# Optimization experiments

Hardware: AMD Instinct MI355X
Metric: run time of the kernel (lower is better)

Reference implementation:

```python
import jax, jax.numpy as jnp
import numpy as np

HEAD_DIM = 256
N_Q = 8
N_KV = 4
HIDDEN = 2304
WINDOW = 1024
SOFT_CAP = 50.0
MAX_WAVELENGTH = 10000.0


def _rope(x, start_index=0):
    # x: [b, s, n, h]. keras_hub RotaryEmbedding (rotate-half convention),
    # followed by Gemma's interleave permutation of the feature dim.
    b, s, n, h = x.shape
    inv_freq = 1.0 / (MAX_WAVELENGTH ** (jnp.arange(0, h, 2, dtype=jnp.float32) / h))
    pos = jnp.arange(s, dtype=jnp.float32) + start_index
    freq = pos[:, None] * inv_freq[None, :]            # [s, h/2]
    emb = jnp.concatenate([freq, freq], axis=-1)[None, :, None, :]  # [1, s, 1, h]
    cos, sin = jnp.cos(emb).astype(x.dtype), jnp.sin(emb).astype(x.dtype)
    x1, x2 = jnp.split(x, 2, axis=-1)
    rot = jnp.concatenate([-x2, x1], axis=-1)
    y = x * cos + rot * sin
    # Gemma _apply_rope: split halves then interleave (same permutation on q and k)
    a, b2 = jnp.split(y, 2, axis=-1)
    return jnp.stack([a, b2], axis=-1).reshape(x.shape)


def setup_inputs() -> dict:
    key = jax.random.key(0)
    ks = jax.random.split(key, 5)
    B, T, D = 2, 2048, HIDDEN
    x = jax.random.normal(ks[0], (B, T, D), dtype=jnp.float32)
    # causal mask [b, q_len, kv_len]
    causal = jnp.tril(jnp.ones((T, T), dtype=bool))
    attention_mask = jnp.broadcast_to(causal[None], (B, T, T))
    scale = 0.02
    Wq = jax.random.normal(ks[1], (N_Q, D, HEAD_DIM), dtype=jnp.float32) * scale
    Wk = jax.random.normal(ks[2], (N_KV, D, HEAD_DIM), dtype=jnp.float32) * scale
    Wv = jax.random.normal(ks[3], (N_KV, D, HEAD_DIM), dtype=jnp.float32) * scale
    Wo = jax.random.normal(ks[4], (N_Q, HEAD_DIM, D), dtype=jnp.float32) * scale
    return {"x": x, "attention_mask": attention_mask, "Wq": Wq, "Wk": Wk, "Wv": Wv, "Wo": Wo}


def reference(x, attention_mask, Wq, Wk, Wv, Wo):
    b, t, d = x.shape
    q = jnp.einsum('btd,ndh->btnh', x, Wq)
    k = jnp.einsum('bsd,kdh->bskh', x, Wk)
    v = jnp.einsum('bsd,kdh->bskh', x, Wv)
    q = _rope(q)
    k = _rope(k)
    s = k.shape[1]
    # sliding window band mask (triu(-w+1) & tril(w-1)), rows sliced at cache_update_index=0
    i = jnp.arange(s)[:, None]
    j = jnp.arange(s)[None, :]
    sliding = (j - i <= WINDOW - 1) & (i - j <= WINDOW - 1)
    mask = attention_mask & sliding[None, :t, :s]      # [b, t, s]
    q = q * jnp.asarray(1.0 / np.sqrt(HEAD_DIM), dtype=q.dtype)
    g = N_Q // N_KV
    qg = q.reshape(b, t, N_KV, g, HEAD_DIM)
    logits = jnp.einsum('btkgh,bskh->bkgts', qg, k).astype(jnp.float32)
    logits = jnp.tanh(logits / SOFT_CAP) * SOFT_CAP    # logit soft-cap
    m = mask[:, None, None, :, :]                      # [b, 1, 1, t, s]
    logits = jnp.where(m, logits, jnp.float32(-1e30))
    probs = jax.nn.softmax(logits, axis=-1).astype(q.dtype)
    out = jnp.einsum('bkgts,bskh->btkgh', probs, v).reshape(b, t, N_Q, HEAD_DIM)
    no_attended = jnp.all(~attention_mask, axis=-1, keepdims=True)[..., None]  # [b, t, 1, 1]
    out = jnp.where(no_attended, jnp.zeros_like(out), out)
    return jnp.einsum('btnh,nhd->btd', out, Wo)
```

## Files before the change

### kernel.cpp

```cpp
#include <hip/hip_runtime.h>
#include <math.h>

#define HEAD_DIM 256
#define N_Q 8
#define N_KV 4
#define HIDDEN 2304
#define WINDOW 1024
#define BATCH 2
#define SEQ 2048
#define BT (BATCH*SEQ)

typedef unsigned short u16;
typedef __attribute__((ext_vector_type(8))) short bf16x8;
typedef __attribute__((ext_vector_type(4))) float f32x4;

__device__ __forceinline__ u16 f2bf(float f) {
    union { float f; unsigned u; } c; c.f = f;
    unsigned r = c.u + 0x7FFF + ((c.u >> 16) & 1);
    return (u16)(r >> 16);
}
__device__ __forceinline__ float bf2f(u16 b) {
    union { float f; unsigned u; } c; c.u = ((unsigned)b) << 16;
    return c.f;
}

__global__ __launch_bounds__(256) void convert_x_kernel(
    const float* __restrict__ x, u16* __restrict__ xb, int n8)
{
    int i = blockIdx.x * 256 + threadIdx.x;
    if (i >= n8) return;
    const float4 a = ((const float4*)x)[2*i];
    const float4 b = ((const float4*)x)[2*i+1];
    u16 o[8] = { f2bf(a.x), f2bf(a.y), f2bf(a.z), f2bf(a.w),
                 f2bf(b.x), f2bf(b.y), f2bf(b.z), f2bf(b.w) };
    ((uint4*)xb)[i] = *(const uint4*)o;
}

__global__ __launch_bounds__(256) void wqkv_t_kernel(
    const float* __restrict__ Wq, const float* __restrict__ Wk,
    const float* __restrict__ Wv, u16* __restrict__ Wt)
{
    __shared__ float t[64][65];
    const int j = blockIdx.z;
    const float* W = (j < 8)  ? Wq + (size_t)j*HIDDEN*HEAD_DIM
                   : (j < 12) ? Wk + (size_t)(j-8)*HIDDEN*HEAD_DIM
                              : Wv + (size_t)(j-12)*HIDDEN*HEAD_DIM;
    const int d0 = blockIdx.x * 64, h0 = blockIdx.y * 64;
    const int tid = threadIdx.x;
    {
        const int r = tid >> 4, c4 = tid & 15;
        #pragma unroll
        for (int rr = r; rr < 64; rr += 16) {
            const float4 v = *(const float4*)(W + (size_t)(d0+rr)*HEAD_DIM + h0 + c4*4);
            t[rr][c4*4+0] = v.x; t[rr][c4*4+1] = v.y;
            t[rr][c4*4+2] = v.z; t[rr][c4*4+3] = v.w;
        }
    }
    __syncthreads();
    {
        const int hh = tid >> 2;
        #pragma unroll
        for (int it = 0; it < 2; it++) {
            const int chunk = (tid & 3) + it*4;
            u16 tmp[8];
            #pragma unroll
            for (int jj = 0; jj < 8; jj++) tmp[jj] = f2bf(t[chunk*8+jj][hh]);
            *(uint4*)&Wt[(size_t)(j*256 + h0 + hh)*HIDDEN + d0 + chunk*8] = *(const uint4*)tmp;
        }
    }
}

__global__ __launch_bounds__(256) void wo_t_kernel(
    const float* __restrict__ Wo, u16* __restrict__ Wot)
{
    __shared__ float t[64][65];
    const int k0 = blockIdx.x * 64, d0 = blockIdx.y * 64;
    const int tid = threadIdx.x;
    {
        const int r = tid >> 4, c4 = tid & 15;
        #pragma unroll
        for (int rr = r; rr < 64; rr += 16) {
            const float4 v = *(const float4*)(Wo + (size_t)(k0+rr)*HIDDEN + d0 + c4*4);
            t[rr][c4*4+0] = v.x; t[rr][c4*4+1] = v.y;
            t[rr][c4*4+2] = v.z; t[rr][c4*4+3] = v.w;
        }
    }
    __syncthreads();
    {
        const int dd = tid >> 2;
        #pragma unroll
        for (int it = 0; it < 2; it++) {
            const int chunk = (tid & 3) + it*4;
            u16 tmp[8];
            #pragma unroll
            for (int jj = 0; jj < 8; jj++) tmp[jj] = f2bf(t[chunk*8+jj][dd]);
            *(uint4*)&Wot[(size_t)(d0 + dd)*(N_Q*HEAD_DIM) + k0 + chunk*8] = *(const uint4*)tmp;
        }
    }
}

template<typename OutT>
__global__ __launch_bounds__(256) void gemm_bf16_kernel(
    const u16* __restrict__ A, const u16* __restrict__ Bt,
    OutT* __restrict__ C, int M, int N, int K)
{
    __shared__ u16 As[128*64];
    __shared__ u16 Bs[128*64];
    const int m0 = blockIdx.y * 128;
    const int n0 = blockIdx.x * 128;
    const int tid  = threadIdx.x;
    const int lane = tid & 63;
    const int wave = tid >> 6;
    const int wm = (wave & 1) * 64;
    const int wn = (wave >> 1) * 64;
    const int l16  = lane & 15;
    const int quad = lane >> 4;

    const int srow8  = lane >> 3;
    const int schunk = (lane & 7) ^ srow8;
    const u16* Ag = A  + (size_t)(m0 + wave*8 + srow8)*K + schunk*8;
    const u16* Bg = Bt + (size_t)(n0 + wave*8 + srow8)*K + schunk*8;

    const int axor = l16 & 7;
    const u16* ArA = As + (wm + l16)*64;
    const u16* BrB = Bs + (wn + l16)*64;

    f32x4 acc[4][4];
    #pragma unroll
    for (int i = 0; i < 4; i++)
        #pragma unroll
        for (int j = 0; j < 4; j++) acc[i][j] = (f32x4){0.f,0.f,0.f,0.f};

    for (int k0 = 0; k0 < K; k0 += 64) {
        __syncthreads();
        #pragma unroll
        for (int c = 0; c < 4; c++) {
            __builtin_amdgcn_global_load_lds(
                (const __attribute__((address_space(1))) unsigned int*)(Ag + (size_t)c*32*K + k0),
                (__attribute__((address_space(3))) unsigned int*)&As[(c*32 + wave*8)*64],
                16, 0, 0);
            __builtin_amdgcn_global_load_lds(
                (const __attribute__((address_space(1))) unsigned int*)(Bg + (size_t)c*32*K + k0),
                (__attribute__((address_space(3))) unsigned int*)&Bs[(c*32 + wave*8)*64],
                16, 0, 0);
        }
        __syncthreads();
        #pragma unroll
        for (int kk = 0; kk < 2; kk++) {
            bf16x8 af[4], bfr[4];
            #pragma unroll
            for (int t = 0; t < 4; t++)
                af[t]  = *(const bf16x8*)(ArA + t*16*64 + (((kk<<2)|quad) ^ axor)*8);
            #pragma unroll
            for (int t = 0; t < 4; t++)
                bfr[t] = *(const bf16x8*)(BrB + t*16*64 + (((kk<<2)|quad) ^ axor)*8);
            #pragma unroll
            for (int i = 0; i < 4; i++)
                #pragma unroll
                for (int j = 0; j < 4; j++)
                    acc[i][j] = __builtin_amdgcn_mfma_f32_16x16x32_bf16(
                                    af[i], bfr[j], acc[i][j], 0, 0, 0);
        }
    }

    #pragma unroll
    for (int i = 0; i < 4; i++) {
        const int rbase = m0 + wm + i*16 + quad*4;
        #pragma unroll
        for (int j = 0; j < 4; j++) {
            const int col = n0 + wn + j*16 + l16;
            #pragma unroll
            for (int r = 0; r < 4; r++) {
                const float v = acc[i][j][r];
                if constexpr (sizeof(OutT) == 2)
                    ((u16*)C)[(size_t)(rbase + r)*N + col] = f2bf(v);
                else
                    ((float*)C)[(size_t)(rbase + r)*N + col] = v;
            }
        }
    }
}

__global__ __launch_bounds__(256) void rope_kernel(
    const u16* __restrict__ raw, u16* __restrict__ qb, u16* __restrict__ kbf)
{
    const int r   = blockIdx.x;
    const int pos = r & (SEQ-1);
    const int tid = threadIdx.x;
    const u16* row = raw + (size_t)r * 4096;
    const float LOG1E4 = 9.210340371976184f;

    #pragma unroll
    for (int p = tid; p < 1024; p += 256) {
        const int n = p >> 7, j = p & 127;
        const float lo = bf2f(row[n*256 + j]);
        const float hi = bf2f(row[n*256 + j + 128]);
        const float inv = __expf(-LOG1E4 * (float)j * (1.0f/128.0f));
        float s, c; sincosf((float)pos * inv, &s, &c);
        qb[((size_t)r*N_Q + n)*HEAD_DIM + j]       = f2bf((lo*c - hi*s) * 0.0625f);
        qb[((size_t)r*N_Q + n)*HEAD_DIM + j + 128] = f2bf((hi*c + lo*s) * 0.0625f);
    }
    #pragma unroll
    for (int p = tid; p < 512; p += 256) {
        const int n = p >> 7, j = p & 127;
        const float lo = bf2f(row[2048 + n*256 + j]);
        const float hi = bf2f(row[2048 + n*256 + j + 128]);
        const float inv = __expf(-LOG1E4 * (float)j * (1.0f/128.0f));
        float s, c; sincosf((float)pos * inv, &s, &c);
        kbf[((size_t)r*N_KV + n)*HEAD_DIM + j]       = f2bf(lo*c - hi*s);
        kbf[((size_t)r*N_KV + n)*HEAD_DIM + j + 128] = f2bf(hi*c + lo*s);
    }
}

__global__ __launch_bounds__(256) void vtrans_kernel(
    const u16* __restrict__ raw, u16* __restrict__ vtt)
{
    __shared__ u16 T[32*264];
    const int blk = blockIdx.x;
    const int sc  = blk & 63;
    const int bk  = blk >> 6;
    const int b   = bk >> 2, kh = bk & 3;
    const int tid = threadIdx.x;

    const u16* rrow = raw + (size_t)(b*SEQ + sc*32)*4096 + 3072 + kh*256;
    {
        const int s = tid >> 3;
        #pragma unroll
        for (int it = 0; it < 4; it++) {
            const int seg = (tid & 7) + it*8;
            *(uint4*)&T[s*264 + seg*8] = *(const uint4*)(rrow + (size_t)s*4096 + seg*8);
        }
    }
    __syncthreads();
    u16* out = vtt + (size_t)blk*8192;
    #pragma unroll
    for (int it = 0; it < 4; it++) {
        const int o = tid + it*256;
        const int h = o >> 2, ss = o & 3;
        u16 tmp[8];
        #pragma unroll
        for (int j = 0; j < 8; j++) tmp[j] = T[(ss*8 + j)*264 + h];
        *(uint4*)(out + h*32 + ((ss ^ (h & 3))*8)) = *(const uint4*)tmp;
    }
}

#define AQT 64
__global__ __launch_bounds__(256) void attn_mfma_kernel(
    const u16* __restrict__ qb, const u16* __restrict__ kb,
    const u16* __restrict__ vtt, u16* __restrict__ ao)
{
    __shared__ u16 Ks[32*264];
    __shared__ u16 Vs[256*32];
    __shared__ u16 Ps[64*40];
    __shared__ float lsum[64];

    const int qh = blockIdx.y;
    const int kh = qh >> 1;
    const int bx = ((blockIdx.y >> 2) & 1) ? (gridDim.x - 1 - (int)blockIdx.x)
                                           : (int)blockIdx.x;
    const int t0 = bx * AQT;
    const int b  = t0 >> 11;
    const int tb = t0 & (SEQ-1);
    const int tid  = threadIdx.x;
    const int wave = tid >> 6;
    const int lane = tid & 63;
    const int l16  = lane & 15;
    const int quad = lane >> 4;

    bf16x8 qf[8];
    {
        const u16* qrow = qb + ((size_t)(t0 + wave*16 + l16)*N_Q + qh)*HEAD_DIM + quad*8;
        #pragma unroll
        for (int c = 0; c < 8; c++) qf[c] = *(const bf16x8*)(qrow + c*32);
    }

    f32x4 o[4][4];
    #pragma unroll
    for (int i = 0; i < 4; i++)
        #pragma unroll
        for (int j = 0; j < 4; j++) o[i][j] = (f32x4){0.f,0.f,0.f,0.f};
    float lpart[4] = {0.f, 0.f, 0.f, 0.f};

    int s_begin = tb - (WINDOW-1); if (s_begin < 0) s_begin = 0;
    const int st0 = s_begin & ~31;

    const u16* kbase = kb  + ((size_t)(b*SEQ)*N_KV + kh)*HEAD_DIM;
    const u16* vbase = vtt + ((size_t)(b*N_KV + kh)*SEQ)*HEAD_DIM;

    for (int st = st0; st < tb + AQT; st += 32) {
        __syncthreads();
        {
            const u16* vtile = vbase + (size_t)st*HEAD_DIM;
            #pragma unroll
            for (int c = 0; c < 4; c++) {
                const int off = wave*2048 + c*512;
                __builtin_amdgcn_global_load_lds(
                    (const __attribute__((address_space(1))) unsigned int*)(vtile + off + lane*8),
                    (__attribute__((address_space(3))) unsigned int*)&Vs[off],
                    16, 0, 0);
            }
            const int s = tid >> 3;
            const u16* krow = kbase + (size_t)(st + s)*(N_KV*HEAD_DIM);
            #pragma unroll
            for (int it = 0; it < 4; it++) {
                const int seg = (tid & 7) + it*8;
                *(uint4*)&Ks[s*264 + seg*8] = *(const uint4*)(krow + seg*8);
            }
        }
        __syncthreads();

        f32x4 sc[2];
        #pragma unroll
        for (int sf = 0; sf < 2; sf++) {
            f32x4 a = (f32x4){0.f,0.f,0.f,0.f};
            const u16* kr = &Ks[(sf*16 + l16)*264 + quad*8];
            #pragma unroll
            for (int c = 0; c < 8; c++)
                a = __builtin_amdgcn_mfma_f32_16x16x32_bf16(
                        qf[c], *(const bf16x8*)(kr + c*32), a, 0, 0, 0);
            sc[sf] = a;
        }

        #pragma unroll
        for (int sf = 0; sf < 2; sf++) {
            const int sg = st + sf*16 + l16;
            #pragma unroll
            for (int r = 0; r < 4; r++) {
                const int tg = tb + wave*16 + quad*4 + r;
                const float e1 = __expf(sc[sf][r] * 0.04f);
                float p = __expf(-100.0f / (e1 + 1.0f));
                const bool ok = (sg <= tg) && (tg - sg < WINDOW);
                p = ok ? p : 0.0f;
                lpart[r] += p;
                Ps[(wave*16 + quad*4 + r)*40 + sf*16 + l16] = f2bf(p);
            }
        }
        __syncthreads();

        bf16x8 ap[4];
        #pragma unroll
        for (int i = 0; i < 4; i++)
            ap[i] = *(const bf16x8*)&Ps[(i*16 + l16)*40 + quad*8];
        #pragma unroll
        for (int j = 0; j < 4; j++) {
            const int hr = wave*64 + j*16 + l16;
            const bf16x8 bv = *(const bf16x8*)&Vs[hr*32 + ((quad ^ (l16 & 3))*8)];
            #pragma unroll
            for (int i = 0; i < 4; i++)
                o[i][j] = __builtin_amdgcn_mfma_f32_16x16x32_bf16(ap[i], bv, o[i][j], 0, 0, 0);
        }
    }

    #pragma unroll
    for (int r = 0; r < 4; r++) {
        float s = lpart[r];
        #pragma unroll
        for (int sh = 1; sh <= 8; sh <<= 1) s += __shfl_xor(s, sh, 64);
        if (l16 == 0) lsum[wave*16 + quad*4 + r] = s;
    }
    __syncthreads();

    #pragma unroll
    for (int i = 0; i < 4; i++) {
        #pragma unroll
        for (int r = 0; r < 4; r++) {
            const int rl  = i*16 + quad*4 + r;
            const float inv = 1.0f / (lsum[rl] + 1e-30f);
            u16* arow = ao + ((size_t)(t0 + rl)*N_Q + qh)*HEAD_DIM + wave*64 + l16;
            #pragma unroll
            for (int j = 0; j < 4; j++)
                arow[j*16] = f2bf(o[i][j][r] * inv);
        }
    }
}

extern "C" void kernel_launch(void* const* d_in, const int* in_sizes, int n_in,
                              void* d_out, int out_size, void* d_ws, size_t ws_size,
                              hipStream_t stream)
{
    const float* x  = (const float*)d_in[0];
    const float* Wq = (const float*)d_in[2];
    const float* Wk = (const float*)d_in[3];
    const float* Wv = (const float*)d_in[4];
    const float* Wo = (const float*)d_in[5];
    float* out = (float*)d_out;

    char* w = (char*)d_ws;
    u16* qbuf = (u16*)(w);
    u16* kbuf = (u16*)(w +  16777216ull);
    u16* vtt  = (u16*)(w +  25165824ull);
    u16* aob  = (u16*)(w +  33554432ull);
    u16* xb   = (u16*)(w +  50331648ull);
    u16* wt1  = (u16*)(w +  69206016ull);
    u16* wot  = (u16*)(w +  88080384ull);
    u16* raw  = (u16*)(w +  97517568ull);

    const int n8 = BT*HIDDEN/8;
    convert_x_kernel<<<(n8+255)/256, 256, 0, stream>>>(x, xb, n8);
    wqkv_t_kernel<<<dim3(HIDDEN/64, HEAD_DIM/64, 16), 256, 0, stream>>>(Wq, Wk, Wv, wt1);
    wo_t_kernel<<<dim3(N_Q*HEAD_DIM/64, HIDDEN/64), 256, 0, stream>>>(Wo, wot);

    gemm_bf16_kernel<u16><<<dim3(4096/128, BT/128), 256, 0, stream>>>(
        xb, wt1, raw, BT, 4096, HIDDEN);
    rope_kernel<<<BT, 256, 0, stream>>>(raw, qbuf, kbuf);
    vtrans_kernel<<<BATCH*N_KV*64, 256, 0, stream>>>(raw, vtt);
    attn_mfma_kernel<<<dim3(BT/AQT, N_Q), 256, 0, stream>>>(qbuf, kbuf, vtt, aob);
    gemm_bf16_kernel<float><<<dim3(HIDDEN/128, BT/128), 256, 0, stream>>>(
        aob, wot, out, BT, HIDDEN, N_Q*HEAD_DIM);
}
```

Baseline: 415.4 us.

## Merge prep kernels, fuse V transpose into QKV GEMM, restructure attention PV

Folds the x conversion and both weight-transpose kernels into one prep launch. The QKV GEMM epilogue now writes the V columns straight into the swizzled transposed V layout, which removes the separate vtrans kernel and its read back of raw. The attention kernel changes the PV MFMA so each wave owns its 16 query rows across all 256 head dims. This drops a __syncthreads and the shared lsum reduction, at the cost of 16 accumulators per wave and scattered epilogue stores. RoPE switches to the fast __sincosf, which loses some accuracy for large angles.

```diff
diff --git a/kernel.cpp b/kernel.cpp
--- a/kernel.cpp
+++ b/kernel.cpp
@@ -24,30 +24,36 @@
     return c.f;
 }
 
-__global__ __launch_bounds__(256) void convert_x_kernel(
-    const float* __restrict__ x, u16* __restrict__ xb, int n8)
-{
-    int i = blockIdx.x * 256 + threadIdx.x;
-    if (i >= n8) return;
-    const float4 a = ((const float4*)x)[2*i];
-    const float4 b = ((const float4*)x)[2*i+1];
-    u16 o[8] = { f2bf(a.x), f2bf(a.y), f2bf(a.z), f2bf(a.w),
-                 f2bf(b.x), f2bf(b.y), f2bf(b.z), f2bf(b.w) };
-    ((uint4*)xb)[i] = *(const uint4*)o;
-}
-
-__global__ __launch_bounds__(256) void wqkv_t_kernel(
+#define PREP_X_BLK   4608
+#define PREP_W1_BLK  2304
+__global__ __launch_bounds__(256) void prep_kernel(
+    const float* __restrict__ x,
     const float* __restrict__ Wq, const float* __restrict__ Wk,
-    const float* __restrict__ Wv, u16* __restrict__ Wt)
+    const float* __restrict__ Wv, const float* __restrict__ Wo,
+    u16* __restrict__ xb, u16* __restrict__ Wt, u16* __restrict__ Wot)
 {
     __shared__ float t[64][65];
-    const int j = blockIdx.z;
-    const float* W = (j < 8)  ? Wq + (size_t)j*HIDDEN*HEAD_DIM
-                   : (j < 12) ? Wk + (size_t)(j-8)*HIDDEN*HEAD_DIM
-                              : Wv + (size_t)(j-12)*HIDDEN*HEAD_DIM;
-    const int d0 = blockIdx.x * 64, h0 = blockIdx.y * 64;
+    const int bid = blockIdx.x;
     const int tid = threadIdx.x;
-    {
+
+    if (bid < PREP_X_BLK) {
+        const int i = bid * 256 + tid;
+        const float4 a = ((const float4*)x)[2*i];
+        const float4 b = ((const float4*)x)[2*i+1];
+        u16 o[8] = { f2bf(a.x), f2bf(a.y), f2bf(a.z), f2bf(a.w),
+                     f2bf(b.x), f2bf(b.y), f2bf(b.z), f2bf(b.w) };
+        ((uint4*)xb)[i] = *(const uint4*)o;
+        return;
+    }
+    if (bid < PREP_X_BLK + PREP_W1_BLK) {
+        const int local = bid - PREP_X_BLK;
+        const int j   = local / 144;
+        const int rem = local % 144;
+        const int d0  = (rem % 36) * 64;
+        const int h0  = (rem / 36) * 64;
+        const float* W = (j < 8)  ? Wq + (size_t)j*HIDDEN*HEAD_DIM
+                       : (j < 12) ? Wk + (size_t)(j-8)*HIDDEN*HEAD_DIM
+                                  : Wv + (size_t)(j-12)*HIDDEN*HEAD_DIM;
         const int r = tid >> 4, c4 = tid & 15;
         #pragma unroll
         for (int rr = r; rr < 64; rr += 16) {
@@ -55,9 +61,7 @@
             t[rr][c4*4+0] = v.x; t[rr][c4*4+1] = v.y;
             t[rr][c4*4+2] = v.z; t[rr][c4*4+3] = v.w;
         }
-    }
-    __syncthreads();
-    {
+        __syncthreads();
         const int hh = tid >> 2;
         #pragma unroll
         for (int it = 0; it < 2; it++) {
@@ -67,16 +71,12 @@
             for (int jj = 0; jj < 8; jj++) tmp[jj] = f2bf(t[chunk*8+jj][hh]);
             *(uint4*)&Wt[(size_t)(j*256 + h0 + hh)*HIDDEN + d0 + chunk*8] = *(const uint4*)tmp;
         }
-    }
-}
-
-__global__ __launch_bounds__(256) void wo_t_kernel(
-    const float* __restrict__ Wo, u16* __restrict__ Wot)
-{
-    __shared__ float t[64][65];
-    const int k0 = blockIdx.x * 64, d0 = blockIdx.y * 64;
-    const int tid = threadIdx.x;
+        return;
+    }
     {
+        const int local = bid - PREP_X_BLK - PREP_W1_BLK;
+        const int k0 = (local % 32) * 64;
+        const int d0 = (local / 32) * 64;
         const int r = tid >> 4, c4 = tid & 15;
         #pragma unroll
         for (int rr = r; rr < 64; rr += 16) {
@@ -84,9 +84,7 @@
             t[rr][c4*4+0] = v.x; t[rr][c4*4+1] = v.y;
             t[rr][c4*4+2] = v.z; t[rr][c4*4+3] = v.w;
         }
-    }
-    __syncthreads();
-    {
+        __syncthreads();
         const int dd = tid >> 2;
         #pragma unroll
         for (int it = 0; it < 2; it++) {
@@ -102,7 +100,7 @@
 template<typename OutT>
 __global__ __launch_bounds__(256) void gemm_bf16_kernel(
     const u16* __restrict__ A, const u16* __restrict__ Bt,
-    OutT* __restrict__ C, int M, int N, int K)
+    OutT* __restrict__ C, u16* __restrict__ vtt, int M, int N, int K)
 {
     __shared__ u16 As[128*64];
     __shared__ u16 Bs[128*64];
@@ -163,6 +161,28 @@
         }
     }
 
+    if (sizeof(OutT) == 2 && n0 >= 3072) {
+        #pragma unroll
+        for (int i = 0; i < 4; i++) {
+            const int rbase = m0 + wm + i*16 + quad*4;
+            #pragma unroll
+            for (int j = 0; j < 4; j++) {
+                const int gcol = n0 + wn + j*16 + l16 - 3072;
+                const int kh = gcol >> 8, h = gcol & 255;
+                #pragma unroll
+                for (int r = 0; r < 4; r++) {
+                    const int row = rbase + r;
+                    const int bb = row >> 11, sq = row & (SEQ-1);
+                    const int tile = (bb*N_KV + kh)*64 + (sq >> 5);
+                    const int ss = sq & 31;
+                    vtt[(size_t)tile*8192 + h*32 + (((ss>>3) ^ (h&3))*8) + (ss&7)]
+                        = f2bf(acc[i][j][r]);
+                }
+            }
+        }
+        return;
+    }
+
     #pragma unroll
     for (int i = 0; i < 4; i++) {
         const int rbase = m0 + wm + i*16 + quad*4;
@@ -196,7 +216,7 @@
         const float lo = bf2f(row[n*256 + j]);
         const float hi = bf2f(row[n*256 + j + 128]);
         const float inv = __expf(-LOG1E4 * (float)j * (1.0f/128.0f));
-        float s, c; sincosf((float)pos * inv, &s, &c);
+        float s, c; __sincosf((float)pos * inv, &s, &c);
         qb[((size_t)r*N_Q + n)*HEAD_DIM + j]       = f2bf((lo*c - hi*s) * 0.0625f);
         qb[((size_t)r*N_Q + n)*HEAD_DIM + j + 128] = f2bf((hi*c + lo*s) * 0.0625f);
     }
@@ -206,41 +226,9 @@
         const float lo = bf2f(row[2048 + n*256 + j]);
         const float hi = bf2f(row[2048 + n*256 + j + 128]);
         const float inv = __expf(-LOG1E4 * (float)j * (1.0f/128.0f));
-        float s, c; sincosf((float)pos * inv, &s, &c);
+        float s, c; __sincosf((float)pos * inv, &s, &c);
         kbf[((size_t)r*N_KV + n)*HEAD_DIM + j]       = f2bf(lo*c - hi*s);
         kbf[((size_t)r*N_KV + n)*HEAD_DIM + j + 128] = f2bf(hi*c + lo*s);
-    }
-}
-
-__global__ __launch_bounds__(256) void vtrans_kernel(
-    const u16* __restrict__ raw, u16* __restrict__ vtt)
-{
-    __shared__ u16 T[32*264];
-    const int blk = blockIdx.x;
-    const int sc  = blk & 63;
-    const int bk  = blk >> 6;
-    const int b   = bk >> 2, kh = bk & 3;
-    const int tid = threadIdx.x;
-
-    const u16* rrow = raw + (size_t)(b*SEQ + sc*32)*4096 + 3072 + kh*256;
-    {
-        const int s = tid >> 3;
-        #pragma unroll
-        for (int it = 0; it < 4; it++) {
-            const int seg = (tid & 7) + it*8;
-            *(uint4*)&T[s*264 + seg*8] = *(const uint4*)(rrow + (size_t)s*4096 + seg*8);
-        }
-    }
-    __syncthreads();
-    u16* out = vtt + (size_t)blk*8192;
-    #pragma unroll
-    for (int it = 0; it < 4; it++) {
-        const int o = tid + it*256;
-        const int h = o >> 2, ss = o & 3;
-        u16 tmp[8];
-        #pragma unroll
-        for (int j = 0; j < 8; j++) tmp[j] = T[(ss*8 + j)*264 + h];
-        *(uint4*)(out + h*32 + ((ss ^ (h & 3))*8)) = *(const uint4*)tmp;
     }
 }
 
@@ -252,7 +240,6 @@
     __shared__ u16 Ks[32*264];
     __shared__ u16 Vs[256*32];
     __shared__ u16 Ps[64*40];
-    __shared__ float lsum[64];
 
     const int qh = blockIdx.y;
     const int kh = qh >> 1;
@@ -274,11 +261,9 @@
         for (int c = 0; c < 8; c++) qf[c] = *(const bf16x8*)(qrow + c*32);
     }
 
-    f32x4 o[4][4];
-    #pragma unroll
-    for (int i = 0; i < 4; i++)
-        #pragma unroll
-        for (int j = 0; j < 4; j++) o[i][j] = (f32x4){0.f,0.f,0.f,0.f};
+    f32x4 o[16];
+    #pragma unroll
+    for (int n = 0; n < 16; n++) o[n] = (f32x4){0.f,0.f,0.f,0.f};
     float lpart[4] = {0.f, 0.f, 0.f, 0.f};
 
     int s_begin = tb - (WINDOW-1); if (s_begin < 0) s_begin = 0;
@@ -335,42 +320,31 @@
                 Ps[(wave*16 + quad*4 + r)*40 + sf*16 + l16] = f2bf(p);
             }
         }
-        __syncthreads();
-
-        bf16x8 ap[4];
-        #pragma unroll
-        for (int i = 0; i < 4; i++)
-            ap[i] = *(const bf16x8*)&Ps[(i*16 + l16)*40 + quad*8];
-        #pragma unroll
-        for (int j = 0; j < 4; j++) {
-            const int hr = wave*64 + j*16 + l16;
-            const bf16x8 bv = *(const bf16x8*)&Vs[hr*32 + ((quad ^ (l16 & 3))*8)];
-            #pragma unroll
-            for (int i = 0; i < 4; i++)
-                o[i][j] = __builtin_amdgcn_mfma_f32_16x16x32_bf16(ap[i], bv, o[i][j], 0, 0, 0);
-        }
-    }
-
+
+        const bf16x8 ap = *(const bf16x8*)&Ps[(wave*16 + l16)*40 + quad*8];
+        #pragma unroll
+        for (int n = 0; n < 16; n++) {
+            const bf16x8 bv = *(const bf16x8*)&Vs[(n*16 + l16)*32 + ((quad ^ (l16 & 3))*8)];
+            o[n] = __builtin_amdgcn_mfma_f32_16x16x32_bf16(ap, bv, o[n], 0, 0, 0);
+        }
+    }
+
+    float inv[4];
     #pragma unroll
     for (int r = 0; r < 4; r++) {
         float s = lpart[r];
         #pragma unroll
         for (int sh = 1; sh <= 8; sh <<= 1) s += __shfl_xor(s, sh, 64);
-        if (l16 == 0) lsum[wave*16 + quad*4 + r] = s;
-    }
-    __syncthreads();
-
-    #pragma unroll
-    for (int i = 0; i < 4; i++) {
-        #pragma unroll
-        for (int r = 0; r < 4; r++) {
-            const int rl  = i*16 + quad*4 + r;
-            const float inv = 1.0f / (lsum[rl] + 1e-30f);
-            u16* arow = ao + ((size_t)(t0 + rl)*N_Q + qh)*HEAD_DIM + wave*64 + l16;
-            #pragma unroll
-            for (int j = 0; j < 4; j++)
-                arow[j*16] = f2bf(o[i][j][r] * inv);
-        }
+        inv[r] = 1.0f / (s + 1e-30f);
+    }
+
+    #pragma unroll
+    for (int r = 0; r < 4; r++) {
+        const int row = t0 + wave*16 + quad*4 + r;
+        u16* arow = ao + ((size_t)row*N_Q + qh)*HEAD_DIM + l16;
+        #pragma unroll
+        for (int n = 0; n < 16; n++)
+            arow[n*16] = f2bf(o[n][r] * inv[r]);
     }
 }
 
@@ -395,16 +369,13 @@
     u16* wot  = (u16*)(w +  88080384ull);
     u16* raw  = (u16*)(w +  97517568ull);
 
-    const int n8 = BT*HIDDEN/8;
-    convert_x_kernel<<<(n8+255)/256, 256, 0, stream>>>(x, xb, n8);
-    wqkv_t_kernel<<<dim3(HIDDEN/64, HEAD_DIM/64, 16), 256, 0, stream>>>(Wq, Wk, Wv, wt1);
-    wo_t_kernel<<<dim3(N_Q*HEAD_DIM/64, HIDDEN/64), 256, 0, stream>>>(Wo, wot);
+    prep_kernel<<<PREP_X_BLK + PREP_W1_BLK + 1152, 256, 0, stream>>>(
+        x, Wq, Wk, Wv, Wo, xb, wt1, wot);
 
     gemm_bf16_kernel<u16><<<dim3(4096/128, BT/128), 256, 0, stream>>>(
-        xb, wt1, raw, BT, 4096, HIDDEN);
+        xb, wt1, raw, vtt, BT, 4096, HIDDEN);
     rope_kernel<<<BT, 256, 0, stream>>>(raw, qbuf, kbuf);
-    vtrans_kernel<<<BATCH*N_KV*64, 256, 0, stream>>>(raw, vtt);
     attn_mfma_kernel<<<dim3(BT/AQT, N_Q), 256, 0, stream>>>(qbuf, kbuf, vtt, aob);
     gemm_bf16_kernel<float><<<dim3(HIDDEN/128, BT/128), 256, 0, stream>>>(
-        aob, wot, out, BT, HIDDEN, N_Q*HEAD_DIM);
-}
+        aob, wot, out, nullptr, BT, HIDDEN, N_Q*HEAD_DIM);
+}
```

After: 420.0 us. About the same (+1.1%).
